# Kernel optimization log

Hardware: AMD Instinct MI355X
Metric: run time of the kernel (lower is better)

Reference implementation:

```python
import jax, jax.numpy as jnp
import numpy as np

N = 20000      # interaction nodes
E = 160000     # edges
NU = 100000    # num_users
NI = 100000    # num_items
EMB = 64       # emb_size
L1, L2 = 256, 128  # GCN layer dims
H = 2          # GAT heads (and number of GAT layers)
EPS = 1e-5


def _seg(x, idx, n):
    return jax.ops.segment_sum(x, idx, num_segments=n)


def _gcn(x, W, b, src, dst, n):
    # GCNConv: add self-loops, sym-normalize, aggregate src->dst
    loops = jnp.arange(n)
    s = jnp.concatenate([src, loops])
    d = jnp.concatenate([dst, loops])
    deg = _seg(jnp.ones(s.shape[0], x.dtype), d, n)
    dinv = jnp.where(deg > 0, 1.0 / jnp.sqrt(deg), 0.0)
    xw = x @ W
    return _seg((dinv[s] * dinv[d])[:, None] * xw[s], d, n) + b


def _bn(x, g, b):
    # BatchNorm1d in training mode: biased batch statistics
    mu = x.mean(0)
    var = x.var(0)
    return (x - mu) / jnp.sqrt(var + EPS) * g + b


def _sage(x, Wl, bl, Wr, src, dst, n):
    # SAGEConv: mean neighbor aggregation (no self loops) + root transform
    cnt = _seg(jnp.ones(src.shape[0], x.dtype), dst, n)
    agg = _seg(x[src], dst, n) / jnp.maximum(cnt, 1.0)[:, None]
    return agg @ Wl + bl + x @ Wr


def _cheb(x, W0, W1c, b, src, dst, n):
    # ChebConv K=2, lambda_max=2: Tx0 = x, Tx1 = -D^{-1/2} A D^{-1/2} x
    deg = _seg(jnp.ones(src.shape[0], x.dtype), dst, n)
    dinv = jnp.where(deg > 0, 1.0 / jnp.sqrt(deg), 0.0)
    tx1 = -_seg((dinv[src] * dinv[dst])[:, None] * x[src], dst, n)
    return x @ W0 + tx1 @ W1c + b


def _gat(x, W, a_s, a_d, b, src, dst, n):
    # GATConv: add self-loops, per-edge attention softmax over dst, concat=False -> mean over heads
    loops = jnp.arange(n)
    s = jnp.concatenate([src, loops])
    d = jnp.concatenate([dst, loops])
    xp = (x @ W).reshape(n, H, L2)           # [n, H, C]
    al = (xp * a_s).sum(-1)                  # [n, H]
    ar = (xp * a_d).sum(-1)                  # [n, H]
    e = jax.nn.leaky_relu(al[s] + ar[d], 0.2)  # [E', H]
    m = jax.lax.stop_gradient(jax.ops.segment_max(e, d, num_segments=n))
    ex = jnp.exp(e - m[d])
    alpha = ex / _seg(ex, d, n)[d]
    out = _seg(alpha[:, :, None] * xp[s], d, n)  # [n, H, C]
    return out.mean(1) + b


def setup_inputs() -> dict:
    key = jax.random.key(0)
    ks = jax.random.split(key, 40)
    f = lambda k, shp: jax.random.normal(k, shp, dtype=jnp.float32) * 0.02
    inp = {
        'user_idx': jax.random.randint(ks[0], (N,), 0, NU, dtype=jnp.int32),
        'item_idx': jax.random.randint(ks[1], (N,), 0, NI, dtype=jnp.int32),
        'edge_index': jax.random.randint(ks[2], (2, E), 0, N, dtype=jnp.int32),
        'user_emb': f(ks[3], (NU, EMB)),
        'item_emb': f(ks[4], (NI, EMB)),
        'W1': f(ks[5], (2 * EMB, 1024)), 'b1': f(ks[6], (1024,)),
        'W2': f(ks[7], (1024, 512)), 'b2': f(ks[8], (512,)),
        'Wg1': f(ks[9], (512, L1)), 'bg1': f(ks[10], (L1,)),
        'gamma1': 1.0 + f(ks[11], (L1,)), 'beta1': f(ks[12], (L1,)),
        'Wg2': f(ks[13], (L1, L2)), 'bg2': f(ks[14], (L2,)),
        'gamma2': 1.0 + f(ks[15], (L2,)), 'beta2': f(ks[16], (L2,)),
        'Wsl': f(ks[17], (L2, L2)), 'bsl': f(ks[18], (L2,)),
        'Wsr': f(ks[19], (L2, L2)),
        'Wc0': f(ks[20], (L2, L2)), 'Wc1': f(ks[21], (L2, L2)), 'bc': f(ks[22], (L2,)),
        'Wgat1': f(ks[23], (L2, H * L2)), 'as1': f(ks[24], (H, L2)), 'ad1': f(ks[25], (H, L2)), 'bgat1': f(ks[26], (L2,)),
        'Wgat2': f(ks[27], (L2, H * L2)), 'as2': f(ks[28], (H, L2)), 'ad2': f(ks[29], (H, L2)), 'bgat2': f(ks[30], (L2,)),
        'Wp': f(ks[31], (L2, 1)), 'bp': f(ks[32], (1,)),
    }
    return inp


def reference(user_idx, item_idx, edge_index, user_emb, item_emb, W1, b1, W2, b2,
              Wg1, bg1, gamma1, beta1, Wg2, bg2, gamma2, beta2,
              Wsl, bsl, Wsr, Wc0, Wc1, bc,
              Wgat1, as1, ad1, bgat1, Wgat2, as2, ad2, bgat2, Wp, bp):
    src, dst = edge_index[0], edge_index[1]
    n = user_idx.shape[0]
    x = jnp.concatenate([user_emb[user_idx], item_emb[item_idx]], axis=1)
    # MLP (dropout is identity in eval mode)
    x = jax.nn.relu(x @ W1 + b1)
    x = jax.nn.relu(x @ W2 + b2)
    x = jax.nn.relu(_bn(_gcn(x, Wg1, bg1, src, dst, n), gamma1, beta1))
    x = jax.nn.relu(_bn(_gcn(x, Wg2, bg2, src, dst, n), gamma2, beta2))
    x = jax.nn.relu(_sage(x, Wsl, bsl, Wsr, src, dst, n))
    x = jax.nn.relu(_cheb(x, Wc0, Wc1, bc, src, dst, n))
    x = jax.nn.elu(_gat(x, Wgat1, as1, ad1, bgat1, src, dst, n))
    x = jax.nn.elu(_gat(x, Wgat2, as2, ad2, bgat2, src, dst, n))
    return (x @ Wp + bp)[:, 0]
```

## Files before the change

kernel.cpp:

```cpp
#include <hip/hip_runtime.h>
#include <hip/hip_bf16.h>

typedef __hip_bfloat16 bf16;
typedef short s8v __attribute__((ext_vector_type(8)));
typedef float f4v __attribute__((ext_vector_type(4)));

#define NN 20000
#define NE 160000
#define BN_EPS 1e-5f
#define NB 79

#define GF_BIAS 1
#define GF_RELU 2

static __device__ __forceinline__ float b2f(const bf16 x){ return __bfloat162float(x); }
static __device__ __forceinline__ float bits2f(unsigned int u){ return __uint_as_float(u << 16); }
static __device__ __forceinline__ unsigned short f2bits(float f){
  bf16 h = __float2bfloat16(f);
  unsigned short u; __builtin_memcpy(&u, &h, 2); return u;
}
static __device__ __forceinline__ float lrelu(float v){ return (v > 0.f) ? v : 0.2f * v; }

static inline int cdiv(int a, int b){ return (a + b - 1) / b; }

static __device__ __forceinline__ void gload16(const short* g, short* l){
  __builtin_amdgcn_global_load_lds(
      (const __attribute__((address_space(1))) unsigned int*)g,
      (__attribute__((address_space(3))) unsigned int*)l, 16, 0, 0);
}


__global__ void k_chk_bf(const unsigned short* __restrict__ x, int n, int code,
                         int* __restrict__ diag){
  bool bad = false;
  for (int k = blockIdx.x * 256 + threadIdx.x; k < n; k += gridDim.x * 256)
    if ((x[k] & 0x7F80u) == 0x7F80u) bad = true;
  if (bad) atomicCAS(diag, 0, code);
}

__global__ void k_diag_out(const int* __restrict__ diag, float* __restrict__ out){
  int d = *diag;
  if (d == 0) return;
  int i = blockIdx.x * 256 + threadIdx.x;
  if (i < NN) out[i] = (float)(d * 100);
}


__global__ void k_ideg(const int* __restrict__ dst, int* __restrict__ ideg){
  int e = blockIdx.x * 256 + threadIdx.x;
  if (e < NE) atomicAdd(&ideg[dst[e]], 1);
}

__global__ __launch_bounds__(256) void k_scan1(const int* __restrict__ ideg,
                                               int* __restrict__ tmp,
                                               int* __restrict__ bsum){
  __shared__ int lds[256];
  int tid = threadIdx.x;
  int i = blockIdx.x * 256 + tid;
  int v = (i < NN) ? ideg[i] : 0;
  lds[tid] = v;
  __syncthreads();
  for (int off = 1; off < 256; off <<= 1){
    int t = (tid >= off) ? lds[tid - off] : 0;
    __syncthreads();
    lds[tid] += t;
    __syncthreads();
  }
  if (i < NN) tmp[i] = lds[tid];
  if (tid == 255) bsum[blockIdx.x] = lds[255];
}

__global__ __launch_bounds__(128) void k_scan2(const int* __restrict__ bsum,
                                               int* __restrict__ boff){
  __shared__ int lds[128];
  int tid = threadIdx.x;
  int v = (tid < NB) ? bsum[tid] : 0;
  lds[tid] = v;
  __syncthreads();
  for (int off = 1; off < 128; off <<= 1){
    int t = (tid >= off) ? lds[tid - off] : 0;
    __syncthreads();
    lds[tid] += t;
    __syncthreads();
  }
  if (tid < NB) boff[tid] = lds[tid] - v;
}

__global__ __launch_bounds__(256) void k_scan3(const int* __restrict__ ideg,
                                               const int* __restrict__ boff,
                                               int* __restrict__ rowptr,
                                               int* __restrict__ cursor,
                                               float* __restrict__ dg,
                                               float* __restrict__ dc,
                                               float* __restrict__ ic){
  int i = blockIdx.x * 256 + threadIdx.x;
  if (i == 0) rowptr[NN] = NE;
  if (i >= NN) return;
  int v = ideg[i];
  int excl = cursor[i] - v + boff[blockIdx.x];
  rowptr[i] = excl;
  cursor[i] = excl;
  float d = (float)v;
  dg[i] = rsqrtf(d + 1.0f);
  dc[i] = (d > 0.f) ? rsqrtf(d) : 0.f;
  ic[i] = 1.0f / fmaxf(d, 1.0f);
}

__global__ void k_fill(const int* __restrict__ src, const int* __restrict__ dst,
                       int* __restrict__ cursor, int* __restrict__ colsrc){
  int e = blockIdx.x * 256 + threadIdx.x;
  if (e >= NE) return;
  int pos = atomicAdd(&cursor[dst[e]], 1);
  colsrc[pos] = src[e];
}


struct WtPack {
  const float* W[10]; short* hi[10]; short* lo[10];
  int K[10]; int nshift[10]; int base[11];
};

__global__ __launch_bounds__(256) void k_wtall(WtPack p){
  int idx = blockIdx.x * 256 + threadIdx.x;
  if (idx >= p.base[10]) return;
  int seg = 0;
#pragma unroll
  for (int i = 1; i < 10; i++) seg += (idx >= p.base[i]) ? 1 : 0;
  int local = idx - p.base[seg];
  int K = p.K[seg], ns = p.nshift[seg];
  int n = local & ((1 << ns) - 1), k = local >> ns;
  float w = p.W[seg][local];
  unsigned short h = f2bits(w);
  unsigned short l = f2bits(w - bits2f(h));
  p.hi[seg][(size_t)n * K + k] = (short)h;
  p.lo[seg][(size_t)n * K + k] = (short)l;
}


__global__ void k_gather(const int* __restrict__ uidx, const int* __restrict__ iidx,
                         const float* __restrict__ ue, const float* __restrict__ ie,
                         bf16* __restrict__ x0){
  int idx = blockIdx.x * 256 + threadIdx.x;
  if (idx >= NN * 128) return;
  int i = idx >> 7, c = idx & 127;
  float v = (c < 64) ? ue[(size_t)uidx[i] * 64 + c] : ie[(size_t)iidx[i] * 64 + (c - 64)];
  x0[idx] = __float2bfloat16(v);
}


__global__ __launch_bounds__(256) void k_mm64(
    const bf16* A0, const short* B0h, const short* B0l, int K0,
    const bf16* A1, const short* B1h, const short* B1l, int K1,
    const float* __restrict__ bias, bf16* __restrict__ C,
    int M, int Ncol, int flags, int npass){
  __shared__ short As[64][72];
  __shared__ short Bhs[64][72];
  __shared__ short Bls[64][72];
  const int tid = threadIdx.x;
  const int bid = blockIdx.y * gridDim.x + blockIdx.x;
  const int total = gridDim.x * gridDim.y;
  const int L = (bid & 7) * (total >> 3) + (bid >> 3);
  const int row0 = (L / gridDim.x) * 64, col0 = (L % gridDim.x) * 64;
  if (row0 >= M) return;
  const int wid = tid >> 6, lane = tid & 63;
  const int wr = (wid >> 1) * 32, wc = (wid & 1) * 32;
  const int lr = lane & 15, lq = lane >> 4;
  const int sr = tid >> 2, sq = (tid & 3) * 16;

  f4v acc[2][2];
#pragma unroll
  for (int i = 0; i < 2; i++)
#pragma unroll
    for (int j = 0; j < 2; j++)
      acc[i][j] = f4v{0.f, 0.f, 0.f, 0.f};

  const bf16* Aarr[2] = {A0, A1};
  const short* Bharr[2] = {B0h, B1h};
  const short* Blarr[2] = {B0l, B1l};
  const int Karr[2] = {K0, K1};

  const bool arow_ok = (row0 + sr) < M;

  for (int p = 0; p < npass; p++){
    const short* A = (const short*)Aarr[p];
    const short* Bh = Bharr[p];
    const short* Bl = Blarr[p];
    const int K = Karr[p];
    const short* arow = A + (size_t)(row0 + sr) * K + sq;
    const short* bhrow = Bh + (size_t)(col0 + sr) * K + sq;
    const short* blrow = Bl + (size_t)(col0 + sr) * K + sq;

    uint4 ra0 = make_uint4(0,0,0,0), ra1 = make_uint4(0,0,0,0);
    if (arow_ok){ ra0 = *(const uint4*)(arow); ra1 = *(const uint4*)(arow + 8); }
    uint4 rb0 = *(const uint4*)(bhrow), rb1 = *(const uint4*)(bhrow + 8);
    uint4 rc0 = *(const uint4*)(blrow), rc1 = *(const uint4*)(blrow + 8);

    for (int k0 = 0; k0 < K; k0 += 64){
      *(uint4*)&As[sr][sq] = ra0;  *(uint4*)&As[sr][sq + 8] = ra1;
      *(uint4*)&Bhs[sr][sq] = rb0; *(uint4*)&Bhs[sr][sq + 8] = rb1;
      *(uint4*)&Bls[sr][sq] = rc0; *(uint4*)&Bls[sr][sq + 8] = rc1;
      __syncthreads();
      if (k0 + 64 < K){
        int off = k0 + 64;
        if (arow_ok){ ra0 = *(const uint4*)(arow + off); ra1 = *(const uint4*)(arow + off + 8); }
        rb0 = *(const uint4*)(bhrow + off); rb1 = *(const uint4*)(bhrow + off + 8);
        rc0 = *(const uint4*)(blrow + off); rc1 = *(const uint4*)(blrow + off + 8);
      }
#pragma unroll
      for (int t = 0; t < 2; t++){
        s8v a[2], bh2[2], bl2[2];
#pragma unroll
        for (int i = 0; i < 2; i++) a[i] = *(const s8v*)&As[wr + i * 16 + lr][t * 32 + lq * 8];
#pragma unroll
        for (int j = 0; j < 2; j++){
          bh2[j] = *(const s8v*)&Bhs[wc + j * 16 + lr][t * 32 + lq * 8];
          bl2[j] = *(const s8v*)&Bls[wc + j * 16 + lr][t * 32 + lq * 8];
        }
#pragma unroll
        for (int i = 0; i < 2; i++)
#pragma unroll
          for (int j = 0; j < 2; j++){
            acc[i][j] = __builtin_amdgcn_mfma_f32_16x16x32_bf16(a[i], bh2[j], acc[i][j], 0, 0, 0);
            acc[i][j] = __builtin_amdgcn_mfma_f32_16x16x32_bf16(a[i], bl2[j], acc[i][j], 0, 0, 0);
          }
      }
      __syncthreads();
    }
  }

#pragma unroll
  for (int i = 0; i < 2; i++){
#pragma unroll
    for (int rg = 0; rg < 4; rg++){
      int row = row0 + wr + i * 16 + lq * 4 + rg;
      if (row >= M) continue;
#pragma unroll
      for (int j = 0; j < 2; j++){
        int col = col0 + wc + j * 16 + lr;
        float v = acc[i][j][rg];
        if (flags & GF_BIAS) v += bias[col];
        if (flags & GF_RELU) v = fmaxf(v, 0.f);
        C[(size_t)row * Ncol + col] = __float2bfloat16(v);
      }
    }
  }
}


__global__ __launch_bounds__(256) void k_mmw(
    const bf16* A0, const short* B0h, const short* B0l, int K,
    const float* __restrict__ bias, bf16* __restrict__ C,
    int M, int Ncol, int flags){
  __shared__ short As[128 * 64];
  __shared__ short Bhs[64 * 64];
  __shared__ short Bls[64 * 64];
  const int tid = threadIdx.x;
  const int bid = blockIdx.y * gridDim.x + blockIdx.x;
  const int total = gridDim.x * gridDim.y;
  const int L = (bid & 7) * (total >> 3) + (bid >> 3);
  const int row0 = (L / gridDim.x) * 128, col0 = (L % gridDim.x) * 64;
  if (row0 >= M) return;
  const int wid = tid >> 6, lane = tid & 63;
  const int wr2 = (wid >> 1) * 64, wc2 = (wid & 1) * 32;
  const int lr = lane & 15, lq = lane >> 4;

  f4v acc[4][2];
#pragma unroll
  for (int i = 0; i < 4; i++)
#pragma unroll
    for (int j = 0; j < 2; j++)
      acc[i][j] = f4v{0.f, 0.f, 0.f, 0.f};

  const short* A = (const short*)A0;
  const short* asrc[4]; int adst[4];
#pragma unroll
  for (int i = 0; i < 4; i++){
    int ci = i * 256 + tid;
    int r = ci >> 3, sg = ci & 7;
    int ar = row0 + r; if (ar > M - 1) ar = M - 1;
    asrc[i] = A + (size_t)ar * K + sg * 8;
    adst[i] = ci * 8;
  }
  const short* bhsrc[2]; const short* blsrc[2]; int bdst[2];
#pragma unroll
  for (int i = 0; i < 2; i++){
    int ci = i * 256 + tid;
    int r = ci >> 3, sg = ci & 7;
    bhsrc[i] = B0h + (size_t)(col0 + r) * K + sg * 8;
    blsrc[i] = B0l + (size_t)(col0 + r) * K + sg * 8;
    bdst[i] = ci * 8;
  }

  for (int k0 = 0; k0 < K; k0 += 64){
    __syncthreads();
#pragma unroll
    for (int i = 0; i < 4; i++) gload16(asrc[i] + k0, As + adst[i]);
#pragma unroll
    for (int i = 0; i < 2; i++){
      gload16(bhsrc[i] + k0, Bhs + bdst[i]);
      gload16(blsrc[i] + k0, Bls + bdst[i]);
    }
    __syncthreads();
#pragma unroll
    for (int t = 0; t < 2; t++){
      s8v a[4], bh2[2], bl2[2];
#pragma unroll
      for (int i = 0; i < 4; i++)
        a[i] = *(const s8v*)&As[(wr2 + i * 16 + lr) * 64 + t * 32 + lq * 8];
#pragma unroll
      for (int j = 0; j < 2; j++){
        bh2[j] = *(const s8v*)&Bhs[(wc2 + j * 16 + lr) * 64 + t * 32 + lq * 8];
        bl2[j] = *(const s8v*)&Bls[(wc2 + j * 16 + lr) * 64 + t * 32 + lq * 8];
      }
#pragma unroll
      for (int i = 0; i < 4; i++)
#pragma unroll
        for (int j = 0; j < 2; j++){
          acc[i][j] = __builtin_amdgcn_mfma_f32_16x16x32_bf16(a[i], bh2[j], acc[i][j], 0, 0, 0);
          acc[i][j] = __builtin_amdgcn_mfma_f32_16x16x32_bf16(a[i], bl2[j], acc[i][j], 0, 0, 0);
        }
    }
  }

#pragma unroll
  for (int i = 0; i < 4; i++){
#pragma unroll
    for (int rg = 0; rg < 4; rg++){
      int row = row0 + wr2 + i * 16 + lq * 4 + rg;
      if (row >= M) continue;
#pragma unroll
      for (int j = 0; j < 2; j++){
        int col = col0 + wc2 + j * 16 + lr;
        float v = acc[i][j][rg];
        if (flags & GF_BIAS) v += bias[col];
        if (flags & GF_RELU) v = fmaxf(v, 0.f);
        C[(size_t)row * Ncol + col] = __float2bfloat16(v);
      }
    }
  }
}


__global__ __launch_bounds__(256) void k_agg(
    const int* __restrict__ rowptr, const int* __restrict__ colsrc,
    const bf16* __restrict__ x, const float* __restrict__ wn,
    const float* __restrict__ icv, const float* __restrict__ bias,
    float* __restrict__ outf, bf16* __restrict__ outb,
    int qshift, int mode){
  int idx = blockIdx.x * 256 + threadIdx.x;
  int total = NN << qshift;
  if (idx >= total) return;
  int d = idx >> qshift, q = idx & ((1 << qshift) - 1);
  int F = 4 << qshift;
  int c = q * 4;
  int r0 = rowptr[d], r1 = rowptr[d + 1];
  float s0 = 0.f, s1 = 0.f, s2 = 0.f, s3 = 0.f;
  const short* xs = (const short*)x;
  for (int r = r0; r < r1; r += 4){
    int n = r1 - r;
    int i0 = colsrc[r];
    int i1 = (n > 1) ? colsrc[r + 1] : 0;
    int i2 = (n > 2) ? colsrc[r + 2] : 0;
    int i3 = (n > 3) ? colsrc[r + 3] : 0;
    float w0 = (mode == 1) ? 1.f : wn[i0];
    float w1 = (n > 1) ? ((mode == 1) ? 1.f : wn[i1]) : 0.f;
    float w2 = (n > 2) ? ((mode == 1) ? 1.f : wn[i2]) : 0.f;
    float w3 = (n > 3) ? ((mode == 1) ? 1.f : wn[i3]) : 0.f;
    uint2 v0 = *(const uint2*)(xs + (size_t)i0 * F + c);
    uint2 v1 = *(const uint2*)(xs + (size_t)i1 * F + c);
    uint2 v2 = *(const uint2*)(xs + (size_t)i2 * F + c);
    uint2 v3 = *(const uint2*)(xs + (size_t)i3 * F + c);
    s0 += w0 * bits2f(v0.x & 0xffffu) + w1 * bits2f(v1.x & 0xffffu)
        + w2 * bits2f(v2.x & 0xffffu) + w3 * bits2f(v3.x & 0xffffu);
    s1 += w0 * bits2f(v0.x >> 16) + w1 * bits2f(v1.x >> 16)
        + w2 * bits2f(v2.x >> 16) + w3 * bits2f(v3.x >> 16);
    s2 += w0 * bits2f(v0.y & 0xffffu) + w1 * bits2f(v1.y & 0xffffu)
        + w2 * bits2f(v2.y & 0xffffu) + w3 * bits2f(v3.y & 0xffffu);
    s3 += w0 * bits2f(v0.y >> 16) + w1 * bits2f(v1.y >> 16)
        + w2 * bits2f(v2.y >> 16) + w3 * bits2f(v3.y >> 16);
  }
  if (mode == 0){
    float w = wn[d], w2 = w * w;
    uint2 vd = *(const uint2*)(xs + (size_t)d * F + c);
    float4 o;
    o.x = w * s0 + w2 * bits2f(vd.x & 0xffffu) + bias[c + 0];
    o.y = w * s1 + w2 * bits2f(vd.x >> 16)     + bias[c + 1];
    o.z = w * s2 + w2 * bits2f(vd.y & 0xffffu) + bias[c + 2];
    o.w = w * s3 + w2 * bits2f(vd.y >> 16)     + bias[c + 3];
    *(float4*)(outf + (size_t)d * F + c) = o;
  } else {
    float m = (mode == 1) ? icv[d] : -wn[d];
    unsigned int lo = (unsigned int)f2bits(s0 * m) | ((unsigned int)f2bits(s1 * m) << 16);
    unsigned int hi = (unsigned int)f2bits(s2 * m) | ((unsigned int)f2bits(s3 * m) << 16);
    *(uint2*)((short*)outb + (size_t)d * F + c) = make_uint2(lo, hi);
  }
}


__global__ void k_bn_stats(const float* __restrict__ x, float* __restrict__ stats, int F){
  int c = threadIdx.x & (F - 1);
  int rsub = threadIdx.x / F;
  int rpi = 256 / F;
  int r0 = blockIdx.x * 128;
  int rend = min(NN, r0 + 128);
  float s1 = 0.f, s2 = 0.f;
  for (int r = r0 + rsub; r < rend; r += rpi){
    float v = x[(size_t)r * F + c];
    s1 += v; s2 += v * v;
  }
  atomicAdd(&stats[c], s1);
  atomicAdd(&stats[F + c], s2);
}

__global__ void k_bn_apply(const float* __restrict__ x, const float* __restrict__ stats,
                           const float* __restrict__ g, const float* __restrict__ b,
                           int fshift, int total, bf16* __restrict__ out){
  int idx = blockIdx.x * 256 + threadIdx.x;
  if (idx >= total) return;
  int F = 1 << fshift;
  int c = idx & (F - 1);
  float mu = stats[c] * (1.0f / NN);
  float var = fmaxf(stats[F + c] * (1.0f / NN) - mu * mu, 0.f);
  float v = (x[idx] - mu) * rsqrtf(var + BN_EPS) * g[c] + b[c];
  out[idx] = __float2bfloat16(fmaxf(v, 0.f));
}


__global__ __launch_bounds__(256) void k_gat_alar(const bf16* __restrict__ xp,
                                                  const float* __restrict__ as_,
                                                  const float* __restrict__ ad_,
                                                  float* __restrict__ al,
                                                  float* __restrict__ ar){
  int d = blockIdx.x * 4 + (threadIdx.x >> 6);
  int lane = threadIdx.x & 63;
  if (d >= NN) return;
  int c0 = lane * 2;
  unsigned int p0 = *(const unsigned int*)((const short*)xp + (size_t)d * 256 + c0);
  unsigned int p1 = *(const unsigned int*)((const short*)xp + (size_t)d * 256 + 128 + c0);
  float x00 = bits2f(p0 & 0xffffu), x01 = bits2f(p0 >> 16);
  float x10 = bits2f(p1 & 0xffffu), x11 = bits2f(p1 >> 16);
  float sa0 = x00 * as_[c0] + x01 * as_[c0 + 1];
  float sd0 = x00 * ad_[c0] + x01 * ad_[c0 + 1];
  float sa1 = x10 * as_[128 + c0] + x11 * as_[128 + c0 + 1];
  float sd1 = x10 * ad_[128 + c0] + x11 * ad_[128 + c0 + 1];
#pragma unroll
  for (int off = 32; off > 0; off >>= 1){
    sa0 += __shfl_xor(sa0, off); sd0 += __shfl_xor(sd0, off);
    sa1 += __shfl_xor(sa1, off); sd1 += __shfl_xor(sd1, off);
  }
  if (lane == 0){
    al[d * 2] = sa0;     ar[d * 2] = sd0;
    al[d * 2 + 1] = sa1; ar[d * 2 + 1] = sd1;
  }
}

__global__ __launch_bounds__(64) void k_gat(const int* __restrict__ rowptr,
                                            const int* __restrict__ colsrc,
                                            const bf16* __restrict__ xp,
                                            const float* __restrict__ al,
                                            const float* __restrict__ ar,
                                            const float* __restrict__ bias,
                                            bf16* __restrict__ outb,
                                            const float* __restrict__ wp,
                                            const float* __restrict__ bp,
                                            float* __restrict__ outf){
  __shared__ float w0s[64], w1s[64];
  __shared__ int ss[64];
  int d = blockIdx.x;
  int lane = threadIdx.x;
  int r0 = rowptr[d], r1 = rowptr[d + 1];
  float ard0 = ar[d * 2], ard1 = ar[d * 2 + 1];
  float e0 = lrelu(al[d * 2] + ard0);
  float e1 = lrelu(al[d * 2 + 1] + ard1);
  float mx0 = e0, mx1 = e1;
  for (int r = r0 + lane; r < r1; r += 64){
    int s = colsrc[r];
    mx0 = fmaxf(mx0, lrelu(al[s * 2] + ard0));
    mx1 = fmaxf(mx1, lrelu(al[s * 2 + 1] + ard1));
  }
#pragma unroll
  for (int off = 32; off > 0; off >>= 1){
    mx0 = fmaxf(mx0, __shfl_xor(mx0, off));
    mx1 = fmaxf(mx1, __shfl_xor(mx1, off));
  }
  float ps0 = (lane == 0) ? expf(e0 - mx0) : 0.f;
  float ps1 = (lane == 0) ? expf(e1 - mx1) : 0.f;
  for (int r = r0 + lane; r < r1; r += 64){
    int s = colsrc[r];
    ps0 += expf(lrelu(al[s * 2] + ard0) - mx0);
    ps1 += expf(lrelu(al[s * 2 + 1] + ard1) - mx1);
  }
#pragma unroll
  for (int off = 32; off > 0; off >>= 1){
    ps0 += __shfl_xor(ps0, off);
    ps1 += __shfl_xor(ps1, off);
  }
  int c0 = lane * 2;
  float a00, a01, a10, a11;
  {
    float w0 = expf(e0 - mx0), w1 = expf(e1 - mx1);
    unsigned int p0 = *(const unsigned int*)((const short*)xp + (size_t)d * 256 + c0);
    unsigned int p1 = *(const unsigned int*)((const short*)xp + (size_t)d * 256 + 128 + c0);
    a00 = w0 * bits2f(p0 & 0xffffu); a01 = w0 * bits2f(p0 >> 16);
    a10 = w1 * bits2f(p1 & 0xffffu); a11 = w1 * bits2f(p1 >> 16);
  }
  for (int t0 = r0; t0 < r1; t0 += 64){
    int nt = min(64, r1 - t0);
    __syncthreads();
    if (lane < nt){
      int s = colsrc[t0 + lane];
      ss[lane] = s;
      w0s[lane] = expf(lrelu(al[s * 2] + ard0) - mx0);
      w1s[lane] = expf(lrelu(al[s * 2 + 1] + ard1) - mx1);
    }
    __syncthreads();
    for (int r = 0; r < nt; r++){
      int s = ss[r];
      float w0 = w0s[r], w1 = w1s[r];
      unsigned int p0 = *(const unsigned int*)((const short*)xp + (size_t)s * 256 + c0);
      unsigned int p1 = *(const unsigned int*)((const short*)xp + (size_t)s * 256 + 128 + c0);
      a00 += w0 * bits2f(p0 & 0xffffu); a01 += w0 * bits2f(p0 >> 16);
      a10 += w1 * bits2f(p1 & 0xffffu); a11 += w1 * bits2f(p1 >> 16);
    }
  }
  float v0 = 0.5f * (a00 / ps0 + a10 / ps1) + bias[c0];
  float v1 = 0.5f * (a01 / ps0 + a11 / ps1) + bias[c0 + 1];
  v0 = (v0 > 0.f) ? v0 : expm1f(v0);
  v1 = (v1 > 0.f) ? v1 : expm1f(v1);
  if (wp == nullptr){
    unsigned int packed = (unsigned int)f2bits(v0) | ((unsigned int)f2bits(v1) << 16);
    *(unsigned int*)((short*)outb + (size_t)d * 128 + c0) = packed;
  } else {
    float pv = v0 * wp[c0] + v1 * wp[c0 + 1];
#pragma unroll
    for (int off = 32; off > 0; off >>= 1) pv += __shfl_down(pv, off);
    if (lane == 0) outf[d] = pv + bp[0];
  }
}


extern "C" void kernel_launch(void* const* d_in, const int* in_sizes, int n_in,
                              void* d_out, int out_size, void* d_ws, size_t ws_size,
                              hipStream_t stream){
  const int* uidx = (const int*)d_in[0];
  const int* iidx = (const int*)d_in[1];
  const int* eidx = (const int*)d_in[2];
  const int* src = eidx;
  const int* dst = eidx + NE;
  const float* ue  = (const float*)d_in[3];
  const float* ie  = (const float*)d_in[4];
  const float* W1  = (const float*)d_in[5];  const float* b1  = (const float*)d_in[6];
  const float* W2  = (const float*)d_in[7];  const float* b2  = (const float*)d_in[8];
  const float* Wg1 = (const float*)d_in[9];  const float* bg1 = (const float*)d_in[10];
  const float* gamma1 = (const float*)d_in[11]; const float* beta1 = (const float*)d_in[12];
  const float* Wg2 = (const float*)d_in[13]; const float* bg2 = (const float*)d_in[14];
  const float* gamma2 = (const float*)d_in[15]; const float* beta2 = (const float*)d_in[16];
  const float* Wsl = (const float*)d_in[17]; const float* bsl = (const float*)d_in[18];
  const float* Wsr = (const float*)d_in[19];
  const float* Wc0 = (const float*)d_in[20]; const float* Wc1 = (const float*)d_in[21];
  const float* bc  = (const float*)d_in[22];
  const float* Wgat1 = (const float*)d_in[23]; const float* as1 = (const float*)d_in[24];
  const float* ad1 = (const float*)d_in[25];   const float* bgat1 = (const float*)d_in[26];
  const float* Wgat2 = (const float*)d_in[27]; const float* as2 = (const float*)d_in[28];
  const float* ad2 = (const float*)d_in[29];   const float* bgat2 = (const float*)d_in[30];
  const float* Wp  = (const float*)d_in[31];   const float* bp  = (const float*)d_in[32];

  int* diag   = (int*)d_ws;
  int* ideg   = diag + 4;
  float* stats1 = (float*)(ideg + NN);
  float* stats2 = stats1 + 512;
  int* bsum   = (int*)(stats2 + 256);
  int* boff   = bsum + 128;
  int* rowptr = boff + 128;
  int* cursor = rowptr + NN + 4;
  int* colsrc = cursor + NN;
  float* dg = (float*)(colsrc + NE);
  float* dc = dg + NN;
  float* ic = dc + NN;
  float* al = ic + NN;
  float* ar = al + 2 * NN;
  short* w1h = (short*)(ar + 2 * NN);
  short* w1l = w1h + 131072;
  short* w2h = w1l + 131072;
  short* w2l = w2h + 524288;
  short* wg1h = w2l + 524288;
  short* wg1l = wg1h + 131072;
  short* wg2h = wg1l + 131072;
  short* wg2l = wg2h + 32768;
  short* wslh = wg2l + 32768;
  short* wsll = wslh + 16384;
  short* wsrh = wsll + 16384;
  short* wsrl = wsrh + 16384;
  short* wc0h = wsrl + 16384;
  short* wc0l = wc0h + 16384;
  short* wc1h = wc0l + 16384;
  short* wc1l = wc1h + 16384;
  short* wgat1h = wc1l + 16384;
  short* wgat1l = wgat1h + 32768;
  short* wgat2h = wgat1l + 32768;
  short* wgat2l = wgat2h + 32768;
  short* X0 = wgat2l + 32768;
  short* H1 = X0 + (size_t)NN * 128;
  short* H2 = H1 + (size_t)10000 * 1024;

  bf16* x0b  = (bf16*)X0;
  bf16* h1b  = (bf16*)H1;
  bf16* h2b  = (bf16*)H2;
  bf16* xw1b = (bf16*)H1;
  float* g1f = (float*)H2;
  bf16* g1b  = (bf16*)(H1 + (size_t)NN * 256);
  bf16* xw2b = (bf16*)X0;
  float* x3f = (float*)H1;
  bf16* x3b  = (bf16*)H2;
  bf16* aggb = (bf16*)X0;
  bf16* x4b  = (bf16*)(H2 + (size_t)NN * 128);
  bf16* tx1b = (bf16*)X0;
  bf16* x5b  = (bf16*)(H2 + (size_t)NN * 256);
  bf16* xpb  = (bf16*)H1;
  bf16* x6b  = (bf16*)X0;

  auto mm = [&](const bf16* A1, const short* B1h, const short* B1l, int K1,
                const bf16* A2, const short* B2h, const short* B2l, int K2,
                const float* bias, bf16* C, int M, int N, int flags){
    int nx = N / 64;
    int ny = cdiv(M, 64);
    while ((nx * ny) & 7) ny++;
    dim3 g(nx, ny);
    int np = A2 ? 2 : 1;
    k_mm64<<<g, 256, 0, stream>>>(A1, B1h, B1l, K1, A2, B2h, B2l, K2,
                                  bias, C, M, N, flags, np);
  };

  auto mmw = [&](const bf16* A, const short* Bh, const short* Bl, int K,
                 const float* bias, bf16* C, int M, int N, int flags){
    int nx = N / 64;
    int ny = cdiv(M, 128);
    while ((nx * ny) & 7) ny++;
    dim3 g(nx, ny);
    k_mmw<<<g, 256, 0, stream>>>(A, Bh, Bl, K, bias, C, M, N, flags);
  };

  hipMemsetAsync(diag, 0, (size_t)(4 + NN + 768) * 4, stream);

  k_ideg<<<cdiv(NE, 256), 256, 0, stream>>>(dst, ideg);
  k_scan1<<<NB, 256, 0, stream>>>(ideg, cursor, bsum);
  k_scan2<<<1, 128, 0, stream>>>(bsum, boff);
  k_scan3<<<NB, 256, 0, stream>>>(ideg, boff, rowptr, cursor, dg, dc, ic);
  k_fill<<<cdiv(NE, 256), 256, 0, stream>>>(src, dst, cursor, colsrc);

  {
    WtPack p;
    const float* Ws[10] = {W1, W2, Wg1, Wg2, Wsl, Wsr, Wc0, Wc1, Wgat1, Wgat2};
    short* his[10] = {w1h, w2h, wg1h, wg2h, wslh, wsrh, wc0h, wc1h, wgat1h, wgat2h};
    short* los[10] = {w1l, w2l, wg1l, wg2l, wsll, wsrl, wc0l, wc1l, wgat1l, wgat2l};
    int Ks[10] = {128, 1024, 512, 256, 128, 128, 128, 128, 128, 128};
    int nss[10] = {10, 9, 8, 7, 7, 7, 7, 7, 8, 8};
    int off = 0;
    for (int i = 0; i < 10; i++){
      p.W[i] = Ws[i]; p.hi[i] = his[i]; p.lo[i] = los[i];
      p.K[i] = Ks[i]; p.nshift[i] = nss[i]; p.base[i] = off;
      off += Ks[i] << nss[i];
    }
    p.base[10] = off;
    k_wtall<<<cdiv(off, 256), 256, 0, stream>>>(p);
  }

  k_gather<<<cdiv(NN * 128, 256), 256, 0, stream>>>(uidx, iidx, ue, ie, x0b);

  for (int ofs = 0; ofs < NN; ofs += 10000){
    mmw(x0b + (size_t)ofs * 128, w1h, w1l, 128,
        b1, h1b, 10000, 1024, GF_BIAS | GF_RELU);
    mmw(h1b, w2h, w2l, 1024,
        b2, h2b + (size_t)ofs * 512, 10000, 512, GF_BIAS | GF_RELU);
  }

  mmw(h2b, wg1h, wg1l, 512, nullptr, xw1b, NN, 256, 0);
  k_agg<<<cdiv(NN * 64, 256), 256, 0, stream>>>(rowptr, colsrc, xw1b, dg, nullptr, bg1, g1f, nullptr, 6, 0);
  k_bn_stats<<<cdiv(NN, 128), 256, 0, stream>>>(g1f, stats1, 256);
  k_bn_apply<<<cdiv(NN * 256, 256), 256, 0, stream>>>(g1f, stats1, gamma1, beta1, 8, NN * 256, g1b);

  mm(g1b, wg2h, wg2l, 256, nullptr, nullptr, nullptr, 0, nullptr, xw2b, NN, 128, 0);
  k_agg<<<cdiv(NN * 32, 256), 256, 0, stream>>>(rowptr, colsrc, xw2b, dg, nullptr, bg2, x3f, nullptr, 5, 0);
  k_bn_stats<<<cdiv(NN, 128), 256, 0, stream>>>(x3f, stats2, 128);
  k_bn_apply<<<cdiv(NN * 128, 256), 256, 0, stream>>>(x3f, stats2, gamma2, beta2, 7, NN * 128, x3b);

  k_agg<<<cdiv(NN * 32, 256), 256, 0, stream>>>(rowptr, colsrc, x3b, nullptr, ic, nullptr, nullptr, aggb, 5, 1);
  mm(aggb, wslh, wsll, 128, x3b, wsrh, wsrl, 128, bsl, x4b, NN, 128, GF_BIAS | GF_RELU);

  k_agg<<<cdiv(NN * 32, 256), 256, 0, stream>>>(rowptr, colsrc, x4b, dc, nullptr, nullptr, nullptr, tx1b, 5, 2);
  mm(x4b, wc0h, wc0l, 128, tx1b, wc1h, wc1l, 128, bc, x5b, NN, 128, GF_BIAS | GF_RELU);

  mmw(x5b, wgat1h, wgat1l, 128, nullptr, xpb, NN, 256, 0);
  k_gat_alar<<<cdiv(NN, 4), 256, 0, stream>>>(xpb, as1, ad1, al, ar);
  k_gat<<<NN, 64, 0, stream>>>(rowptr, colsrc, xpb, al, ar, bgat1, x6b,
                               nullptr, nullptr, nullptr);
  k_chk_bf<<<256, 256, 0, stream>>>((const unsigned short*)x6b, NN * 128, 16, diag);

  mmw(x6b, wgat2h, wgat2l, 128, nullptr, xpb, NN, 256, 0);
  k_gat_alar<<<cdiv(NN, 4), 256, 0, stream>>>(xpb, as2, ad2, al, ar);
  k_gat<<<NN, 64, 0, stream>>>(rowptr, colsrc, xpb, al, ar, bgat2, nullptr,
                               Wp, bp, (float*)d_out);
  k_diag_out<<<cdiv(NN, 256), 256, 0, stream>>>(diag, (float*)d_out);
}
```

Before: 607.4 us.

## Double-buffer LDS tiles and XOR-swizzle chunks in split-weight GEMM

The k_mmw GEMM now keeps two LDS buffers, so the global-to-LDS loads for the next K tile are issued before the MFMAs on the current tile, and each iteration needs one barrier instead of two. It also XOR-swizzles the 16-byte chunk index by row when loading, to reduce LDS bank conflicts on the fragment reads. This doubles LDS use per block, which may lower occupancy. Correctness relies on gload16 completing before the next barrier.

```diff
diff --git a/kernel.cpp b/kernel.cpp
--- a/kernel.cpp
+++ b/kernel.cpp
@@ -251,9 +251,9 @@
     const bf16* A0, const short* B0h, const short* B0l, int K,
     const float* __restrict__ bias, bf16* __restrict__ C,
     int M, int Ncol, int flags){
-  __shared__ short As[128 * 64];
-  __shared__ short Bhs[64 * 64];
-  __shared__ short Bls[64 * 64];
+  __shared__ short As[2][128 * 64];
+  __shared__ short Bhs[2][64 * 64];
+  __shared__ short Bls[2][64 * 64];
   const int tid = threadIdx.x;
   const int bid = blockIdx.y * gridDim.x + blockIdx.x;
   const int total = gridDim.x * gridDim.y;
@@ -263,6 +263,7 @@
   const int wid = tid >> 6, lane = tid & 63;
   const int wr2 = (wid >> 1) * 64, wc2 = (wid & 1) * 32;
   const int lr = lane & 15, lq = lane >> 4;
+  const int rx = lr & 7;
 
   f4v acc[4][2];
 #pragma unroll
@@ -276,41 +277,56 @@
 #pragma unroll
   for (int i = 0; i < 4; i++){
     int ci = i * 256 + tid;
-    int r = ci >> 3, sg = ci & 7;
+    int r = ci >> 3, c = ci & 7;
     int ar = row0 + r; if (ar > M - 1) ar = M - 1;
-    asrc[i] = A + (size_t)ar * K + sg * 8;
+    asrc[i] = A + (size_t)ar * K + ((c ^ (r & 7)) * 8);
     adst[i] = ci * 8;
   }
   const short* bhsrc[2]; const short* blsrc[2]; int bdst[2];
 #pragma unroll
   for (int i = 0; i < 2; i++){
     int ci = i * 256 + tid;
-    int r = ci >> 3, sg = ci & 7;
-    bhsrc[i] = B0h + (size_t)(col0 + r) * K + sg * 8;
-    blsrc[i] = B0l + (size_t)(col0 + r) * K + sg * 8;
+    int r = ci >> 3, c = ci & 7;
+    int sc = (c ^ (r & 7)) * 8;
+    bhsrc[i] = B0h + (size_t)(col0 + r) * K + sc;
+    blsrc[i] = B0l + (size_t)(col0 + r) * K + sc;
     bdst[i] = ci * 8;
   }
 
-  for (int k0 = 0; k0 < K; k0 += 64){
+  const int nT = K >> 6;
+#pragma unroll
+  for (int i = 0; i < 4; i++) gload16(asrc[i], As[0] + adst[i]);
+#pragma unroll
+  for (int i = 0; i < 2; i++){
+    gload16(bhsrc[i], Bhs[0] + bdst[i]);
+    gload16(blsrc[i], Bls[0] + bdst[i]);
+  }
+
+  int p = 0;
+  for (int t0 = 0; t0 < nT; t0++){
     __syncthreads();
-#pragma unroll
-    for (int i = 0; i < 4; i++) gload16(asrc[i] + k0, As + adst[i]);
-#pragma unroll
-    for (int i = 0; i < 2; i++){
-      gload16(bhsrc[i] + k0, Bhs + bdst[i]);
-      gload16(blsrc[i] + k0, Bls + bdst[i]);
+    if (t0 + 1 < nT){
+      const int kofs = (t0 + 1) << 6;
+      short* Ad = As[p ^ 1]; short* Bhd = Bhs[p ^ 1]; short* Bld = Bls[p ^ 1];
+#pragma unroll
+      for (int i = 0; i < 4; i++) gload16(asrc[i] + kofs, Ad + adst[i]);
+#pragma unroll
+      for (int i = 0; i < 2; i++){
+        gload16(bhsrc[i] + kofs, Bhd + bdst[i]);
+        gload16(blsrc[i] + kofs, Bld + bdst[i]);
+      }
     }
-    __syncthreads();
 #pragma unroll
     for (int t = 0; t < 2; t++){
       s8v a[4], bh2[2], bl2[2];
+      const int ch0 = ((t << 2) | lq) ^ rx;
 #pragma unroll
       for (int i = 0; i < 4; i++)
-        a[i] = *(const s8v*)&As[(wr2 + i * 16 + lr) * 64 + t * 32 + lq * 8];
+        a[i] = *(const s8v*)&As[p][(wr2 + i * 16 + lr) * 64 + ch0 * 8];
 #pragma unroll
       for (int j = 0; j < 2; j++){
-        bh2[j] = *(const s8v*)&Bhs[(wc2 + j * 16 + lr) * 64 + t * 32 + lq * 8];
-        bl2[j] = *(const s8v*)&Bls[(wc2 + j * 16 + lr) * 64 + t * 32 + lq * 8];
+        bh2[j] = *(const s8v*)&Bhs[p][(wc2 + j * 16 + lr) * 64 + ch0 * 8];
+        bl2[j] = *(const s8v*)&Bls[p][(wc2 + j * 16 + lr) * 64 + ch0 * 8];
       }
 #pragma unroll
       for (int i = 0; i < 4; i++)
@@ -320,6 +336,7 @@
           acc[i][j] = __builtin_amdgcn_mfma_f32_16x16x32_bf16(a[i], bl2[j], acc[i][j], 0, 0, 0);
         }
     }
+    p ^= 1;
   }
 
 #pragma unroll
```

Result: slower. 644.8 us (+6.2%).

## Double-buffer split-bf16 GEMM with XOR swizzle; single-pass online softmax in GAT

Applied to the files above, without the earlier changes.

The split-precision GEMM now uses a double-buffered LDS pipeline with 32-wide K tiles. The next tile's global loads are issued before the MFMAs on the current tile, and an XOR swizzle on the LDS layout is meant to reduce bank conflicts. The GAT aggregation kernel drops its separate max and sum passes over the edges and uses an online (running max with rescaling) softmax in a single pass. This saves two rounds of gathers from al and colsrc, at the cost of an extra exp per edge per lane in the inner loop.

```diff
diff --git a/kernel.cpp b/kernel.cpp
--- a/kernel.cpp
+++ b/kernel.cpp
@@ -251,9 +251,9 @@
     const bf16* A0, const short* B0h, const short* B0l, int K,
     const float* __restrict__ bias, bf16* __restrict__ C,
     int M, int Ncol, int flags){
-  __shared__ short As[128 * 64];
-  __shared__ short Bhs[64 * 64];
-  __shared__ short Bls[64 * 64];
+  __shared__ short As[2][128 * 32];
+  __shared__ short Bhs[2][64 * 32];
+  __shared__ short Bls[2][64 * 32];
   const int tid = threadIdx.x;
   const int bid = blockIdx.y * gridDim.x + blockIdx.x;
   const int total = gridDim.x * gridDim.y;
@@ -263,6 +263,8 @@
   const int wid = tid >> 6, lane = tid & 63;
   const int wr2 = (wid >> 1) * 64, wc2 = (wid & 1) * 32;
   const int lr = lane & 15, lq = lane >> 4;
+  const int rx = (lr >> 1) & 3;
+  const int ch = (lq ^ rx) * 8;
 
   f4v acc[4][2];
 #pragma unroll
@@ -272,45 +274,50 @@
       acc[i][j] = f4v{0.f, 0.f, 0.f, 0.f};
 
   const short* A = (const short*)A0;
-  const short* asrc[4]; int adst[4];
-#pragma unroll
-  for (int i = 0; i < 4; i++){
-    int ci = i * 256 + tid;
-    int r = ci >> 3, sg = ci & 7;
-    int ar = row0 + r; if (ar > M - 1) ar = M - 1;
-    asrc[i] = A + (size_t)ar * K + sg * 8;
-    adst[i] = ci * 8;
-  }
-  const short* bhsrc[2]; const short* blsrc[2]; int bdst[2];
+  const short* asrc[2]; int adst[2];
 #pragma unroll
   for (int i = 0; i < 2; i++){
     int ci = i * 256 + tid;
-    int r = ci >> 3, sg = ci & 7;
-    bhsrc[i] = B0h + (size_t)(col0 + r) * K + sg * 8;
-    blsrc[i] = B0l + (size_t)(col0 + r) * K + sg * 8;
-    bdst[i] = ci * 8;
-  }
-
-  for (int k0 = 0; k0 < K; k0 += 64){
+    int r = ci >> 2, c = ci & 3;
+    int ar = row0 + r; if (ar > M - 1) ar = M - 1;
+    asrc[i] = A + (size_t)ar * K + ((c ^ ((r >> 1) & 3)) * 8);
+    adst[i] = ci * 8;
+  }
+  const short* bhsrc; const short* blsrc; int bdst;
+  {
+    int r = tid >> 2, c = tid & 3;
+    int sc = (c ^ ((r >> 1) & 3)) * 8;
+    bhsrc = B0h + (size_t)(col0 + r) * K + sc;
+    blsrc = B0l + (size_t)(col0 + r) * K + sc;
+    bdst = tid * 8;
+  }
+
+  const int nT = K >> 5;
+#pragma unroll
+  for (int i = 0; i < 2; i++) gload16(asrc[i], As[0] + adst[i]);
+  gload16(bhsrc, Bhs[0] + bdst);
+  gload16(blsrc, Bls[0] + bdst);
+
+  int p = 0;
+  for (int t0 = 0; t0 < nT; t0++){
     __syncthreads();
-#pragma unroll
-    for (int i = 0; i < 4; i++) gload16(asrc[i] + k0, As + adst[i]);
-#pragma unroll
-    for (int i = 0; i < 2; i++){
-      gload16(bhsrc[i] + k0, Bhs + bdst[i]);
-      gload16(blsrc[i] + k0, Bls + bdst[i]);
-    }
-    __syncthreads();
-#pragma unroll
-    for (int t = 0; t < 2; t++){
+    if (t0 + 1 < nT){
+      const int kofs = (t0 + 1) << 5;
+      short* Ad = As[p ^ 1]; short* Bhd = Bhs[p ^ 1]; short* Bld = Bls[p ^ 1];
+#pragma unroll
+      for (int i = 0; i < 2; i++) gload16(asrc[i] + kofs, Ad + adst[i]);
+      gload16(bhsrc + kofs, Bhd + bdst);
+      gload16(blsrc + kofs, Bld + bdst);
+    }
+    {
       s8v a[4], bh2[2], bl2[2];
 #pragma unroll
       for (int i = 0; i < 4; i++)
-        a[i] = *(const s8v*)&As[(wr2 + i * 16 + lr) * 64 + t * 32 + lq * 8];
+        a[i] = *(const s8v*)&As[p][(wr2 + i * 16 + lr) * 32 + ch];
 #pragma unroll
       for (int j = 0; j < 2; j++){
-        bh2[j] = *(const s8v*)&Bhs[(wc2 + j * 16 + lr) * 64 + t * 32 + lq * 8];
-        bl2[j] = *(const s8v*)&Bls[(wc2 + j * 16 + lr) * 64 + t * 32 + lq * 8];
+        bh2[j] = *(const s8v*)&Bhs[p][(wc2 + j * 16 + lr) * 32 + ch];
+        bl2[j] = *(const s8v*)&Bls[p][(wc2 + j * 16 + lr) * 32 + ch];
       }
 #pragma unroll
       for (int i = 0; i < 4; i++)
@@ -320,6 +327,7 @@
           acc[i][j] = __builtin_amdgcn_mfma_f32_16x16x32_bf16(a[i], bl2[j], acc[i][j], 0, 0, 0);
         }
     }
+    p ^= 1;
   }
 
 #pragma unroll
@@ -454,6 +462,7 @@
   }
 }
 
+
 __global__ __launch_bounds__(64) void k_gat(const int* __restrict__ rowptr,
                                             const int* __restrict__ colsrc,
                                             const bf16* __restrict__ xp,
@@ -464,7 +473,7 @@
                                             const float* __restrict__ wp,
                                             const float* __restrict__ bp,
                                             float* __restrict__ outf){
-  __shared__ float w0s[64], w1s[64];
+  __shared__ float es0[64], es1[64];
   __shared__ int ss[64];
   int d = blockIdx.x;
   int lane = threadIdx.x;
@@ -472,56 +481,57 @@
   float ard0 = ar[d * 2], ard1 = ar[d * 2 + 1];
   float e0 = lrelu(al[d * 2] + ard0);
   float e1 = lrelu(al[d * 2 + 1] + ard1);
-  float mx0 = e0, mx1 = e1;
-  for (int r = r0 + lane; r < r1; r += 64){
-    int s = colsrc[r];
-    mx0 = fmaxf(mx0, lrelu(al[s * 2] + ard0));
-    mx1 = fmaxf(mx1, lrelu(al[s * 2 + 1] + ard1));
-  }
-#pragma unroll
-  for (int off = 32; off > 0; off >>= 1){
-    mx0 = fmaxf(mx0, __shfl_xor(mx0, off));
-    mx1 = fmaxf(mx1, __shfl_xor(mx1, off));
-  }
-  float ps0 = (lane == 0) ? expf(e0 - mx0) : 0.f;
-  float ps1 = (lane == 0) ? expf(e1 - mx1) : 0.f;
-  for (int r = r0 + lane; r < r1; r += 64){
-    int s = colsrc[r];
-    ps0 += expf(lrelu(al[s * 2] + ard0) - mx0);
-    ps1 += expf(lrelu(al[s * 2 + 1] + ard1) - mx1);
+  float m0 = e0, m1 = e1;
+  float ps0 = (lane == 0) ? 1.f : 0.f;
+  float ps1 = ps0;
+  int c0 = lane * 2;
+  float a00, a01, a10, a11;
+  {
+    unsigned int p0 = *(const unsigned int*)((const short*)xp + (size_t)d * 256 + c0);
+    unsigned int p1 = *(const unsigned int*)((const short*)xp + (size_t)d * 256 + 128 + c0);
+    a00 = bits2f(p0 & 0xffffu); a01 = bits2f(p0 >> 16);
+    a10 = bits2f(p1 & 0xffffu); a11 = bits2f(p1 >> 16);
+  }
+  for (int t0 = r0; t0 < r1; t0 += 64){
+    int nt = min(64, r1 - t0);
+    float el0 = -3.4e38f, el1 = -3.4e38f;
+    int s = 0;
+    if (lane < nt){
+      s = colsrc[t0 + lane];
+      el0 = lrelu(al[s * 2] + ard0);
+      el1 = lrelu(al[s * 2 + 1] + ard1);
+    }
+    __syncthreads();
+    ss[lane] = s; es0[lane] = el0; es1[lane] = el1;
+    __syncthreads();
+    float cm0 = el0, cm1 = el1;
+#pragma unroll
+    for (int off = 32; off > 0; off >>= 1){
+      cm0 = fmaxf(cm0, __shfl_xor(cm0, off));
+      cm1 = fmaxf(cm1, __shfl_xor(cm1, off));
+    }
+    float n0 = fmaxf(m0, cm0), n1 = fmaxf(m1, cm1);
+    float sc0 = expf(m0 - n0), sc1 = expf(m1 - n1);
+    ps0 *= sc0; ps1 *= sc1;
+    a00 *= sc0; a01 *= sc0; a10 *= sc1; a11 *= sc1;
+    m0 = n0; m1 = n1;
+    if (lane < nt){
+      ps0 += expf(el0 - m0);
+      ps1 += expf(el1 - m1);
+    }
+    for (int r = 0; r < nt; r++){
+      int sr_ = ss[r];
+      float w0 = expf(es0[r] - m0), w1 = expf(es1[r] - m1);
+      unsigned int p0 = *(const unsigned int*)((const short*)xp + (size_t)sr_ * 256 + c0);
+      unsigned int p1 = *(const unsigned int*)((const short*)xp + (size_t)sr_ * 256 + 128 + c0);
+      a00 += w0 * bits2f(p0 & 0xffffu); a01 += w0 * bits2f(p0 >> 16);
+      a10 += w1 * bits2f(p1 & 0xffffu); a11 += w1 * bits2f(p1 >> 16);
+    }
   }
 #pragma unroll
   for (int off = 32; off > 0; off >>= 1){
     ps0 += __shfl_xor(ps0, off);
     ps1 += __shfl_xor(ps1, off);
-  }
-  int c0 = lane * 2;
-  float a00, a01, a10, a11;
-  {
-    float w0 = expf(e0 - mx0), w1 = expf(e1 - mx1);
-    unsigned int p0 = *(const unsigned int*)((const short*)xp + (size_t)d * 256 + c0);
-    unsigned int p1 = *(const unsigned int*)((const short*)xp + (size_t)d * 256 + 128 + c0);
-    a00 = w0 * bits2f(p0 & 0xffffu); a01 = w0 * bits2f(p0 >> 16);
-    a10 = w1 * bits2f(p1 & 0xffffu); a11 = w1 * bits2f(p1 >> 16);
-  }
-  for (int t0 = r0; t0 < r1; t0 += 64){
-    int nt = min(64, r1 - t0);
-    __syncthreads();
-    if (lane < nt){
-      int s = colsrc[t0 + lane];
-      ss[lane] = s;
-      w0s[lane] = expf(lrelu(al[s * 2] + ard0) - mx0);
-      w1s[lane] = expf(lrelu(al[s * 2 + 1] + ard1) - mx1);
-    }
-    __syncthreads();
-    for (int r = 0; r < nt; r++){
-      int s = ss[r];
-      float w0 = w0s[r], w1 = w1s[r];
-      unsigned int p0 = *(const unsigned int*)((const short*)xp + (size_t)s * 256 + c0);
-      unsigned int p1 = *(const unsigned int*)((const short*)xp + (size_t)s * 256 + 128 + c0);
-      a00 += w0 * bits2f(p0 & 0xffffu); a01 += w0 * bits2f(p0 >> 16);
-      a10 += w1 * bits2f(p1 & 0xffffu); a11 += w1 * bits2f(p1 >> 16);
-    }
   }
   float v0 = 0.5f * (a00 / ps0 + a10 / ps1) + bias[c0];
   float v1 = 0.5f * (a01 / ps0 + a11 / ps1) + bias[c0 + 1];
```

Measured after the change: 623.7 us. +2.7%, slower.

## Use online softmax in GAT aggregation and run MLP GEMMs unchunked

Applied to the files above, without the earlier changes.

The GAT kernel now computes the softmax max and denominator online while it aggregates, rescaling the running sums per 64-edge tile. This replaces the separate max and sum passes over neighbour attention logits, so colsrc and al are read once per edge instead of three times. The MLP stage now issues single full-size GEMMs over all 20000 rows when the workspace is large enough, falling back to two 10000-row chunks otherwise, which halves the GEMM launches and gives each launch more rows to parallelise over. In exchange the GAT kernel recomputes exp per edge per lane inside the inner loop and adds rescaling work, and the larger H1 buffer needs more workspace.

```diff
diff --git a/kernel.cpp b/kernel.cpp
--- a/kernel.cpp
+++ b/kernel.cpp
@@ -454,6 +454,7 @@
   }
 }
 
+
 __global__ __launch_bounds__(64) void k_gat(const int* __restrict__ rowptr,
                                             const int* __restrict__ colsrc,
                                             const bf16* __restrict__ xp,
@@ -464,7 +465,7 @@
                                             const float* __restrict__ wp,
                                             const float* __restrict__ bp,
                                             float* __restrict__ outf){
-  __shared__ float w0s[64], w1s[64];
+  __shared__ float es0[64], es1[64];
   __shared__ int ss[64];
   int d = blockIdx.x;
   int lane = threadIdx.x;
@@ -472,56 +473,57 @@
   float ard0 = ar[d * 2], ard1 = ar[d * 2 + 1];
   float e0 = lrelu(al[d * 2] + ard0);
   float e1 = lrelu(al[d * 2 + 1] + ard1);
-  float mx0 = e0, mx1 = e1;
-  for (int r = r0 + lane; r < r1; r += 64){
-    int s = colsrc[r];
-    mx0 = fmaxf(mx0, lrelu(al[s * 2] + ard0));
-    mx1 = fmaxf(mx1, lrelu(al[s * 2 + 1] + ard1));
-  }
-#pragma unroll
-  for (int off = 32; off > 0; off >>= 1){
-    mx0 = fmaxf(mx0, __shfl_xor(mx0, off));
-    mx1 = fmaxf(mx1, __shfl_xor(mx1, off));
-  }
-  float ps0 = (lane == 0) ? expf(e0 - mx0) : 0.f;
-  float ps1 = (lane == 0) ? expf(e1 - mx1) : 0.f;
-  for (int r = r0 + lane; r < r1; r += 64){
-    int s = colsrc[r];
-    ps0 += expf(lrelu(al[s * 2] + ard0) - mx0);
-    ps1 += expf(lrelu(al[s * 2 + 1] + ard1) - mx1);
+  float m0 = e0, m1 = e1;
+  float ps0 = (lane == 0) ? 1.f : 0.f;
+  float ps1 = ps0;
+  int c0 = lane * 2;
+  float a00, a01, a10, a11;
+  {
+    unsigned int p0 = *(const unsigned int*)((const short*)xp + (size_t)d * 256 + c0);
+    unsigned int p1 = *(const unsigned int*)((const short*)xp + (size_t)d * 256 + 128 + c0);
+    a00 = bits2f(p0 & 0xffffu); a01 = bits2f(p0 >> 16);
+    a10 = bits2f(p1 & 0xffffu); a11 = bits2f(p1 >> 16);
+  }
+  for (int t0 = r0; t0 < r1; t0 += 64){
+    int nt = min(64, r1 - t0);
+    float el0 = -3.4e38f, el1 = -3.4e38f;
+    int s = 0;
+    if (lane < nt){
+      s = colsrc[t0 + lane];
+      el0 = lrelu(al[s * 2] + ard0);
+      el1 = lrelu(al[s * 2 + 1] + ard1);
+    }
+    __syncthreads();
+    ss[lane] = s; es0[lane] = el0; es1[lane] = el1;
+    __syncthreads();
+    float cm0 = el0, cm1 = el1;
+#pragma unroll
+    for (int off = 32; off > 0; off >>= 1){
+      cm0 = fmaxf(cm0, __shfl_xor(cm0, off));
+      cm1 = fmaxf(cm1, __shfl_xor(cm1, off));
+    }
+    float n0 = fmaxf(m0, cm0), n1 = fmaxf(m1, cm1);
+    float sc0 = expf(m0 - n0), sc1 = expf(m1 - n1);
+    ps0 *= sc0; ps1 *= sc1;
+    a00 *= sc0; a01 *= sc0; a10 *= sc1; a11 *= sc1;
+    m0 = n0; m1 = n1;
+    if (lane < nt){
+      ps0 += expf(el0 - m0);
+      ps1 += expf(el1 - m1);
+    }
+    for (int r = 0; r < nt; r++){
+      int sr_ = ss[r];
+      float w0 = expf(es0[r] - m0), w1 = expf(es1[r] - m1);
+      unsigned int p0 = *(const unsigned int*)((const short*)xp + (size_t)sr_ * 256 + c0);
+      unsigned int p1 = *(const unsigned int*)((const short*)xp + (size_t)sr_ * 256 + 128 + c0);
+      a00 += w0 * bits2f(p0 & 0xffffu); a01 += w0 * bits2f(p0 >> 16);
+      a10 += w1 * bits2f(p1 & 0xffffu); a11 += w1 * bits2f(p1 >> 16);
+    }
   }
 #pragma unroll
   for (int off = 32; off > 0; off >>= 1){
     ps0 += __shfl_xor(ps0, off);
     ps1 += __shfl_xor(ps1, off);
-  }
-  int c0 = lane * 2;
-  float a00, a01, a10, a11;
-  {
-    float w0 = expf(e0 - mx0), w1 = expf(e1 - mx1);
-    unsigned int p0 = *(const unsigned int*)((const short*)xp + (size_t)d * 256 + c0);
-    unsigned int p1 = *(const unsigned int*)((const short*)xp + (size_t)d * 256 + 128 + c0);
-    a00 = w0 * bits2f(p0 & 0xffffu); a01 = w0 * bits2f(p0 >> 16);
-    a10 = w1 * bits2f(p1 & 0xffffu); a11 = w1 * bits2f(p1 >> 16);
-  }
-  for (int t0 = r0; t0 < r1; t0 += 64){
-    int nt = min(64, r1 - t0);
-    __syncthreads();
-    if (lane < nt){
-      int s = colsrc[t0 + lane];
-      ss[lane] = s;
-      w0s[lane] = expf(lrelu(al[s * 2] + ard0) - mx0);
-      w1s[lane] = expf(lrelu(al[s * 2 + 1] + ard1) - mx1);
-    }
-    __syncthreads();
-    for (int r = 0; r < nt; r++){
-      int s = ss[r];
-      float w0 = w0s[r], w1 = w1s[r];
-      unsigned int p0 = *(const unsigned int*)((const short*)xp + (size_t)s * 256 + c0);
-      unsigned int p1 = *(const unsigned int*)((const short*)xp + (size_t)s * 256 + 128 + c0);
-      a00 += w0 * bits2f(p0 & 0xffffu); a01 += w0 * bits2f(p0 >> 16);
-      a10 += w1 * bits2f(p1 & 0xffffu); a11 += w1 * bits2f(p1 >> 16);
-    }
   }
   float v0 = 0.5f * (a00 / ps0 + a10 / ps1) + bias[c0];
   float v1 = 0.5f * (a01 / ps0 + a11 / ps1) + bias[c0 + 1];
@@ -601,7 +603,16 @@
   short* wgat2l = wgat2h + 32768;
   short* X0 = wgat2l + 32768;
   short* H1 = X0 + (size_t)NN * 128;
-  short* H2 = H1 + (size_t)10000 * 1024;
+
+  size_t h1rows = 20000;
+  short* H2 = H1 + h1rows * 1024;
+  {
+    size_t need = (size_t)((char*)(H2 + (size_t)NN * 512) - (char*)d_ws);
+    if (need > ws_size){
+      h1rows = 10000;
+      H2 = H1 + h1rows * 1024;
+    }
+  }
 
   bf16* x0b  = (bf16*)X0;
   bf16* h1b  = (bf16*)H1;
@@ -667,11 +678,16 @@
 
   k_gather<<<cdiv(NN * 128, 256), 256, 0, stream>>>(uidx, iidx, ue, ie, x0b);
 
-  for (int ofs = 0; ofs < NN; ofs += 10000){
-    mmw(x0b + (size_t)ofs * 128, w1h, w1l, 128,
-        b1, h1b, 10000, 1024, GF_BIAS | GF_RELU);
-    mmw(h1b, w2h, w2l, 1024,
-        b2, h2b + (size_t)ofs * 512, 10000, 512, GF_BIAS | GF_RELU);
+  if (h1rows == 20000){
+    mmw(x0b, w1h, w1l, 128, b1, h1b, 20000, 1024, GF_BIAS | GF_RELU);
+    mmw(h1b, w2h, w2l, 1024, b2, h2b, 20000, 512, GF_BIAS | GF_RELU);
+  } else {
+    for (int ofs = 0; ofs < NN; ofs += 10000){
+      mmw(x0b + (size_t)ofs * 128, w1h, w1l, 128,
+          b1, h1b, 10000, 1024, GF_BIAS | GF_RELU);
+      mmw(h1b, w2h, w2l, 1024,
+          b2, h2b + (size_t)ofs * 512, 10000, 512, GF_BIAS | GF_RELU);
+    }
   }
 
   mmw(h2b, wg1h, wg1l, 512, nullptr, xw1b, NN, 256, 0);
```

After: 584.1 us. -3.8%, faster.
